# Kernel tuning notes

Measured on AMD Instinct MI355X. Metric: run time of the kernel, lower is better.

## Reference

```python
import jax, jax.numpy as jnp
import numpy as np

FP8_MAX = 448.0  # torch.finfo(float8_e4m3fn).max
TINY = float(np.finfo(np.float32).tiny)
BN = BK = 128  # block sizes


def _make_fp8_weight(key, N, K):
    """Mirror _create_fp8_weight: per-128x128-block scales, fp8 quantized values."""
    w = jax.random.normal(key, (N, K), jnp.float32) * 0.01
    wb = w.reshape(N // BN, BN, K // BK, BK)
    amax = jnp.abs(wb).max(axis=(1, 3))
    scale_inv = jnp.maximum(amax / FP8_MAX, TINY)  # [N/BN, K/BK]
    wq = (wb / scale_inv[:, None, :, None]).reshape(N, K)
    wq = wq.astype(jnp.float8_e4m3fn).astype(jnp.float32)  # fp8-rounded values
    return wq, scale_inv


def _dequant(wq, scale_inv):
    N, K = wq.shape
    nb, kb = scale_inv.shape
    wb = wq.reshape(nb, N // nb, kb, K // kb) * scale_inv[:, None, :, None]
    return wb.reshape(N, K)


def setup_inputs() -> dict:
    key = jax.random.key(0)
    kx, k1, k2, k3 = jax.random.split(key, 4)
    T, H, F = 4096, 2048, 7168  # tokens, hidden_dim, ffn_dim
    x = jax.random.normal(kx, (T, H), jnp.float32)
    w1_q, w1_s = _make_fp8_weight(k1, F, H)
    w3_q, w3_s = _make_fp8_weight(k3, F, H)
    w2_q, w2_s = _make_fp8_weight(k2, H, F)
    return {"hidden_states": x, "w1_q": w1_q, "w1_s": w1_s,
            "w3_q": w3_q, "w3_s": w3_s, "w2_q": w2_q, "w2_s": w2_s}


def reference(hidden_states, w1_q, w1_s, w3_q, w3_s, w2_q, w2_s):
    x = hidden_states
    w1 = _dequant(w1_q, w1_s)  # [F, H]
    w3 = _dequant(w3_q, w3_s)  # [F, H]
    w2 = _dequant(w2_q, w2_s)  # [H, F]
    g = x @ w1.T               # [T, F]
    u = x @ w3.T               # [T, F]
    fused = jax.nn.silu(g) * u
    return fused @ w2.T        # [T, H]
```

## Files before the change

### kernel.cpp

```cpp
#include <hip/hip_runtime.h>
#include <stdint.h>

typedef __attribute__((ext_vector_type(8))) short short8;
typedef __attribute__((ext_vector_type(4))) float floatx4;

__device__ __forceinline__ unsigned short f2bf(float f) {
  union { float f; unsigned int u; } c; c.f = f;
  unsigned int u = c.u;
  unsigned int r = (u + 0x7fffu + ((u >> 16) & 1u)) >> 16;
  return (unsigned short)r;
}
__device__ __forceinline__ float bf2f(unsigned short h) {
  union { unsigned int u; float f; } c; c.u = ((unsigned int)h) << 16;
  return c.f;
}

__device__ __forceinline__ void load16_to_lds(const void* g, void* l) {
  __builtin_amdgcn_global_load_lds(
      (const __attribute__((address_space(1))) unsigned int*)g,
      (__attribute__((address_space(3))) unsigned int*)l, 16, 0, 0);
}

__global__ void f32_to_bf16_kernel(const float* __restrict__ in,
                                   unsigned short* __restrict__ out, long n4) {
  long i = blockIdx.x * (long)blockDim.x + threadIdx.x;
  if (i >= n4) return;
  float4 v = ((const float4*)in)[i];
  ushort4 o;
  o.x = f2bf(v.x); o.y = f2bf(v.y); o.z = f2bf(v.z); o.w = f2bf(v.w);
  ((ushort4*)out)[i] = o;
}

__global__ void dequant2_kernel(const float* __restrict__ w1q,
                                const float* __restrict__ s1,
                                const float* __restrict__ w3q,
                                const float* __restrict__ s3,
                                unsigned short* __restrict__ o1,
                                unsigned short* __restrict__ o3,
                                int K, int sK) {
  int n = blockIdx.y;
  int k = blockIdx.x * 1024 + threadIdx.x * 4;
  size_t idx = (size_t)n * K + k;
  int sidx = (n >> 7) * sK + (k >> 7);
  float sc1 = s1[sidx], sc3 = s3[sidx];
  float4 v1 = *(const float4*)(w1q + idx);
  float4 v3 = *(const float4*)(w3q + idx);
  ushort4 a, b;
  a.x = f2bf(v1.x * sc1); a.y = f2bf(v1.y * sc1);
  a.z = f2bf(v1.z * sc1); a.w = f2bf(v1.w * sc1);
  b.x = f2bf(v3.x * sc3); b.y = f2bf(v3.y * sc3);
  b.z = f2bf(v3.z * sc3); b.w = f2bf(v3.w * sc3);
  *(ushort4*)(o1 + idx) = a;
  *(ushort4*)(o3 + idx) = b;
}

__global__ void dequant1_kernel(const float* __restrict__ wq,
                                const float* __restrict__ s,
                                unsigned short* __restrict__ out,
                                int K, int sK) {
  int n = blockIdx.y;
  int k = blockIdx.x * 1024 + threadIdx.x * 4;
  size_t idx = (size_t)n * K + k;
  float sc = s[(n >> 7) * sK + (k >> 7)];
  float4 v = *(const float4*)(wq + idx);
  ushort4 o;
  o.x = f2bf(v.x * sc); o.y = f2bf(v.y * sc);
  o.z = f2bf(v.z * sc); o.w = f2bf(v.w * sc);
  *(ushort4*)(out + idx) = o;
}


__global__ __launch_bounds__(512, 4) void dual_gemm_silu(
    const unsigned short* __restrict__ A,
    const unsigned short* __restrict__ B1,
    const unsigned short* __restrict__ B3,
    unsigned short* __restrict__ C,
    int M, int N, int K) {
  __shared__ unsigned short As[128 * 64];
  __shared__ unsigned short B1s[128 * 64];
  __shared__ unsigned short B3s[128 * 64];

  const int tid = threadIdx.x;
  const int lane = tid & 63;
  const int wave = tid >> 6;
  const int wm = wave >> 2;
  const int wn = wave & 3;
  const int m0 = blockIdx.y * 128, n0 = blockIdx.x * 128;

  const int s0 = tid, s1 = tid + 512;
  const int r0 = s0 >> 3, c0 = ((s0 & 7) ^ (r0 & 7)) * 8;
  const int r1 = s1 >> 3, c1 = ((s1 & 7) ^ (r1 & 7)) * 8;

  const int q = lane >> 4;
  const int r16 = lane & 15;
  const int rx = r16 & 7;

  floatx4 acc_g[4][2], acc_u[4][2];
#pragma unroll
  for (int i = 0; i < 4; i++)
#pragma unroll
    for (int j = 0; j < 2; j++) {
      acc_g[i][j] = (floatx4){0.f, 0.f, 0.f, 0.f};
      acc_u[i][j] = (floatx4){0.f, 0.f, 0.f, 0.f};
    }

  const unsigned short* ag0 = A + (size_t)(m0 + r0) * K + c0;
  const unsigned short* ag1 = A + (size_t)(m0 + r1) * K + c1;
  const unsigned short* b1g0 = B1 + (size_t)(n0 + r0) * K + c0;
  const unsigned short* b1g1 = B1 + (size_t)(n0 + r1) * K + c1;
  const unsigned short* b3g0 = B3 + (size_t)(n0 + r0) * K + c0;
  const unsigned short* b3g1 = B3 + (size_t)(n0 + r1) * K + c1;

  for (int k0 = 0; k0 < K; k0 += 64) {
    load16_to_lds(ag0 + k0, &As[s0 * 8]);
    load16_to_lds(ag1 + k0, &As[s1 * 8]);
    load16_to_lds(b1g0 + k0, &B1s[s0 * 8]);
    load16_to_lds(b1g1 + k0, &B1s[s1 * 8]);
    load16_to_lds(b3g0 + k0, &B3s[s0 * 8]);
    load16_to_lds(b3g1 + k0, &B3s[s1 * 8]);
    __syncthreads();

#pragma unroll
    for (int kh = 0; kh < 2; kh++) {
      const int kq = kh * 4 + q;
      short8 a[4], b1v[2], b3v[2];
#pragma unroll
      for (int t = 0; t < 4; t++) {
        int row = wm * 64 + t * 16 + r16;
        a[t] = *(const short8*)&As[(row * 8 + (kq ^ rx)) * 8];
      }
#pragma unroll
      for (int j = 0; j < 2; j++) {
        int row = wn * 32 + j * 16 + r16;
        int u = (row * 8 + (kq ^ rx)) * 8;
        b1v[j] = *(const short8*)&B1s[u];
        b3v[j] = *(const short8*)&B3s[u];
      }
#pragma unroll
      for (int i = 0; i < 4; i++)
#pragma unroll
        for (int j = 0; j < 2; j++) {
          acc_g[i][j] = __builtin_amdgcn_mfma_f32_16x16x32_bf16(
              a[i], b1v[j], acc_g[i][j], 0, 0, 0);
          acc_u[i][j] = __builtin_amdgcn_mfma_f32_16x16x32_bf16(
              a[i], b3v[j], acc_u[i][j], 0, 0, 0);
        }
    }
    __syncthreads();
  }

#pragma unroll
  for (int i = 0; i < 4; i++) {
    int row0 = m0 + wm * 64 + i * 16 + q * 4;
#pragma unroll
    for (int j = 0; j < 2; j++) {
      int col = n0 + wn * 32 + j * 16 + r16;
#pragma unroll
      for (int rr = 0; rr < 4; rr++) {
        float gv = acc_g[i][j][rr];
        float uv = acc_u[i][j][rr];
        float sv = gv / (1.f + __expf(-gv)) * uv;
        C[(size_t)(row0 + rr) * N + col] = f2bf(sv);
      }
    }
  }
}

__global__ __launch_bounds__(512, 4) void gemm_nt_f32_8w(
    const unsigned short* __restrict__ A,
    const unsigned short* __restrict__ B,
    float* __restrict__ C,
    int M, int N, int K) {
  __shared__ unsigned short As[128 * 64];
  __shared__ unsigned short Bs[128 * 64];

  const int tid = threadIdx.x;
  const int lane = tid & 63;
  const int wave = tid >> 6;
  const int wm = wave >> 2;
  const int wn = wave & 3;
  const int m0 = blockIdx.y * 128, n0 = blockIdx.x * 128;

  const int s0 = tid, s1 = tid + 512;
  const int r0 = s0 >> 3, c0 = ((s0 & 7) ^ (r0 & 7)) * 8;
  const int r1 = s1 >> 3, c1 = ((s1 & 7) ^ (r1 & 7)) * 8;

  const int q = lane >> 4;
  const int r16 = lane & 15;
  const int rx = r16 & 7;

  floatx4 acc[4][2];
#pragma unroll
  for (int i = 0; i < 4; i++)
#pragma unroll
    for (int j = 0; j < 2; j++) acc[i][j] = (floatx4){0.f, 0.f, 0.f, 0.f};

  const unsigned short* ag0 = A + (size_t)(m0 + r0) * K + c0;
  const unsigned short* ag1 = A + (size_t)(m0 + r1) * K + c1;
  const unsigned short* bg0 = B + (size_t)(n0 + r0) * K + c0;
  const unsigned short* bg1 = B + (size_t)(n0 + r1) * K + c1;

  for (int k0 = 0; k0 < K; k0 += 64) {
    load16_to_lds(ag0 + k0, &As[s0 * 8]);
    load16_to_lds(ag1 + k0, &As[s1 * 8]);
    load16_to_lds(bg0 + k0, &Bs[s0 * 8]);
    load16_to_lds(bg1 + k0, &Bs[s1 * 8]);
    __syncthreads();

#pragma unroll
    for (int kh = 0; kh < 2; kh++) {
      const int kq = kh * 4 + q;
      short8 a[4], b[2];
#pragma unroll
      for (int t = 0; t < 4; t++) {
        int row = wm * 64 + t * 16 + r16;
        a[t] = *(const short8*)&As[(row * 8 + (kq ^ rx)) * 8];
      }
#pragma unroll
      for (int j = 0; j < 2; j++) {
        int row = wn * 32 + j * 16 + r16;
        b[j] = *(const short8*)&Bs[(row * 8 + (kq ^ rx)) * 8];
      }
#pragma unroll
      for (int i = 0; i < 4; i++)
#pragma unroll
        for (int j = 0; j < 2; j++)
          acc[i][j] = __builtin_amdgcn_mfma_f32_16x16x32_bf16(
              a[i], b[j], acc[i][j], 0, 0, 0);
    }
    __syncthreads();
  }

#pragma unroll
  for (int i = 0; i < 4; i++) {
    int row0 = m0 + wm * 64 + i * 16 + q * 4;
#pragma unroll
    for (int j = 0; j < 2; j++) {
      int col = n0 + wn * 32 + j * 16 + r16;
#pragma unroll
      for (int rr = 0; rr < 4; rr++)
        C[(size_t)(row0 + rr) * N + col] = acc[i][j][rr];
    }
  }
}

extern "C" void kernel_launch(void* const* d_in, const int* in_sizes, int n_in,
                              void* d_out, int out_size, void* d_ws, size_t ws_size,
                              hipStream_t stream) {
  const float* x = (const float*)d_in[0];
  const float* w1q = (const float*)d_in[1];
  const float* w1s = (const float*)d_in[2];
  const float* w3q = (const float*)d_in[3];
  const float* w3s = (const float*)d_in[4];
  const float* w2q = (const float*)d_in[5];
  const float* w2s = (const float*)d_in[6];

  const int T = 4096, H = 2048, F = 7168;

  char* ws = (char*)d_ws;
  unsigned short* xb  = (unsigned short*)ws;  ws += (size_t)T * H * 2;
  unsigned short* w1b = (unsigned short*)ws;  ws += (size_t)F * H * 2;
  unsigned short* w3b = (unsigned short*)ws;  ws += (size_t)F * H * 2;
  unsigned short* w2b = (unsigned short*)ws;  ws += (size_t)H * F * 2;
  unsigned short* g   = (unsigned short*)ws;  ws += (size_t)T * F * 2;

  long xn4 = (long)T * H / 4;

  f32_to_bf16_kernel<<<(xn4 + 255) / 256, 256, 0, stream>>>(x, xb, xn4);
  dequant2_kernel<<<dim3(H / 1024, F), 256, 0, stream>>>(
      w1q, w1s, w3q, w3s, w1b, w3b, H, H / 128);
  dequant1_kernel<<<dim3(F / 1024, H), 256, 0, stream>>>(
      w2q, w2s, w2b, F, F / 128);

  dual_gemm_silu<<<dim3(F / 128, T / 128), 512, 0, stream>>>(xb, w1b, w3b, g, T, F, H);

  gemm_nt_f32_8w<<<dim3(H / 128, T / 128), 512, 0, stream>>>(g, w2b, (float*)d_out, T, H, F);
}
```

Before: 573.7 us.

## Use 4 waves per block with 64x64 warp tiles in both GEMMs

Both GEMM kernels drop from 8 waves to 4 waves per 128x128 block, so each wave computes a 64x64 sub-tile instead of 64x32. That doubles the MFMA work per B-fragment LDS read and cuts total LDS read traffic per block. Each thread now issues four global-to-LDS loads per matrix, using precomputed offsets. The cost is more accumulator registers per thread (32 floatx4 in the dual GEMM) and fewer waves per block to hide latency, with launch bounds lowered to 256 threads and 2 blocks.

```diff
diff --git a/kernel.cpp b/kernel.cpp
--- a/kernel.cpp
+++ b/kernel.cpp
@@ -70,7 +70,7 @@
 }
 
 
-__global__ __launch_bounds__(512, 4) void dual_gemm_silu(
+__global__ __launch_bounds__(256, 2) void dual_gemm_silu(
     const unsigned short* __restrict__ A,
     const unsigned short* __restrict__ B1,
     const unsigned short* __restrict__ B3,
@@ -83,55 +83,59 @@
   const int tid = threadIdx.x;
   const int lane = tid & 63;
   const int wave = tid >> 6;
-  const int wm = wave >> 2;
-  const int wn = wave & 3;
+  const int wm = wave >> 1;
+  const int wn = wave & 1;
   const int m0 = blockIdx.y * 128, n0 = blockIdx.x * 128;
 
-  const int s0 = tid, s1 = tid + 512;
-  const int r0 = s0 >> 3, c0 = ((s0 & 7) ^ (r0 & 7)) * 8;
-  const int r1 = s1 >> 3, c1 = ((s1 & 7) ^ (r1 & 7)) * 8;
+  int soff[4];
+  int sdst[4];
+#pragma unroll
+  for (int p = 0; p < 4; p++) {
+    int u = tid + 256 * p;
+    int r = u >> 3;
+    int c = ((u & 7) ^ (r & 7)) * 8;
+    soff[p] = r * K + c;
+    sdst[p] = u * 8;
+  }
 
   const int q = lane >> 4;
   const int r16 = lane & 15;
   const int rx = r16 & 7;
 
-  floatx4 acc_g[4][2], acc_u[4][2];
+  floatx4 acc_g[4][4], acc_u[4][4];
 #pragma unroll
   for (int i = 0; i < 4; i++)
 #pragma unroll
-    for (int j = 0; j < 2; j++) {
+    for (int j = 0; j < 4; j++) {
       acc_g[i][j] = (floatx4){0.f, 0.f, 0.f, 0.f};
       acc_u[i][j] = (floatx4){0.f, 0.f, 0.f, 0.f};
     }
 
-  const unsigned short* ag0 = A + (size_t)(m0 + r0) * K + c0;
-  const unsigned short* ag1 = A + (size_t)(m0 + r1) * K + c1;
-  const unsigned short* b1g0 = B1 + (size_t)(n0 + r0) * K + c0;
-  const unsigned short* b1g1 = B1 + (size_t)(n0 + r1) * K + c1;
-  const unsigned short* b3g0 = B3 + (size_t)(n0 + r0) * K + c0;
-  const unsigned short* b3g1 = B3 + (size_t)(n0 + r1) * K + c1;
+  const unsigned short* Abase = A + (size_t)m0 * K;
+  const unsigned short* B1base = B1 + (size_t)n0 * K;
+  const unsigned short* B3base = B3 + (size_t)n0 * K;
 
   for (int k0 = 0; k0 < K; k0 += 64) {
-    load16_to_lds(ag0 + k0, &As[s0 * 8]);
-    load16_to_lds(ag1 + k0, &As[s1 * 8]);
-    load16_to_lds(b1g0 + k0, &B1s[s0 * 8]);
-    load16_to_lds(b1g1 + k0, &B1s[s1 * 8]);
-    load16_to_lds(b3g0 + k0, &B3s[s0 * 8]);
-    load16_to_lds(b3g1 + k0, &B3s[s1 * 8]);
+#pragma unroll
+    for (int p = 0; p < 4; p++) {
+      load16_to_lds(Abase + soff[p] + k0, &As[sdst[p]]);
+      load16_to_lds(B1base + soff[p] + k0, &B1s[sdst[p]]);
+      load16_to_lds(B3base + soff[p] + k0, &B3s[sdst[p]]);
+    }
     __syncthreads();
 
 #pragma unroll
     for (int kh = 0; kh < 2; kh++) {
       const int kq = kh * 4 + q;
-      short8 a[4], b1v[2], b3v[2];
+      short8 a[4], b1v[4], b3v[4];
 #pragma unroll
       for (int t = 0; t < 4; t++) {
         int row = wm * 64 + t * 16 + r16;
         a[t] = *(const short8*)&As[(row * 8 + (kq ^ rx)) * 8];
       }
 #pragma unroll
-      for (int j = 0; j < 2; j++) {
-        int row = wn * 32 + j * 16 + r16;
+      for (int j = 0; j < 4; j++) {
+        int row = wn * 64 + j * 16 + r16;
         int u = (row * 8 + (kq ^ rx)) * 8;
         b1v[j] = *(const short8*)&B1s[u];
         b3v[j] = *(const short8*)&B3s[u];
@@ -139,7 +143,7 @@
 #pragma unroll
       for (int i = 0; i < 4; i++)
 #pragma unroll
-        for (int j = 0; j < 2; j++) {
+        for (int j = 0; j < 4; j++) {
           acc_g[i][j] = __builtin_amdgcn_mfma_f32_16x16x32_bf16(
               a[i], b1v[j], acc_g[i][j], 0, 0, 0);
           acc_u[i][j] = __builtin_amdgcn_mfma_f32_16x16x32_bf16(
@@ -153,8 +157,8 @@
   for (int i = 0; i < 4; i++) {
     int row0 = m0 + wm * 64 + i * 16 + q * 4;
 #pragma unroll
-    for (int j = 0; j < 2; j++) {
-      int col = n0 + wn * 32 + j * 16 + r16;
+    for (int j = 0; j < 4; j++) {
+      int col = n0 + wn * 64 + j * 16 + r16;
 #pragma unroll
       for (int rr = 0; rr < 4; rr++) {
         float gv = acc_g[i][j][rr];
@@ -166,7 +170,7 @@
   }
 }
 
-__global__ __launch_bounds__(512, 4) void gemm_nt_f32_8w(
+__global__ __launch_bounds__(256, 2) void gemm_nt_f32_4w(
     const unsigned short* __restrict__ A,
     const unsigned short* __restrict__ B,
     float* __restrict__ C,
@@ -177,54 +181,59 @@
   const int tid = threadIdx.x;
   const int lane = tid & 63;
   const int wave = tid >> 6;
-  const int wm = wave >> 2;
-  const int wn = wave & 3;
+  const int wm = wave >> 1;
+  const int wn = wave & 1;
   const int m0 = blockIdx.y * 128, n0 = blockIdx.x * 128;
 
-  const int s0 = tid, s1 = tid + 512;
-  const int r0 = s0 >> 3, c0 = ((s0 & 7) ^ (r0 & 7)) * 8;
-  const int r1 = s1 >> 3, c1 = ((s1 & 7) ^ (r1 & 7)) * 8;
+  int soff[4], sdst[4];
+#pragma unroll
+  for (int p = 0; p < 4; p++) {
+    int u = tid + 256 * p;
+    int r = u >> 3;
+    int c = ((u & 7) ^ (r & 7)) * 8;
+    soff[p] = r * K + c;
+    sdst[p] = u * 8;
+  }
 
   const int q = lane >> 4;
   const int r16 = lane & 15;
   const int rx = r16 & 7;
 
-  floatx4 acc[4][2];
+  floatx4 acc[4][4];
 #pragma unroll
   for (int i = 0; i < 4; i++)
 #pragma unroll
-    for (int j = 0; j < 2; j++) acc[i][j] = (floatx4){0.f, 0.f, 0.f, 0.f};
-
-  const unsigned short* ag0 = A + (size_t)(m0 + r0) * K + c0;
-  const unsigned short* ag1 = A + (size_t)(m0 + r1) * K + c1;
-  const unsigned short* bg0 = B + (size_t)(n0 + r0) * K + c0;
-  const unsigned short* bg1 = B + (size_t)(n0 + r1) * K + c1;
+    for (int j = 0; j < 4; j++) acc[i][j] = (floatx4){0.f, 0.f, 0.f, 0.f};
+
+  const unsigned short* Abase = A + (size_t)m0 * K;
+  const unsigned short* Bbase = B + (size_t)n0 * K;
 
   for (int k0 = 0; k0 < K; k0 += 64) {
-    load16_to_lds(ag0 + k0, &As[s0 * 8]);
-    load16_to_lds(ag1 + k0, &As[s1 * 8]);
-    load16_to_lds(bg0 + k0, &Bs[s0 * 8]);
-    load16_to_lds(bg1 + k0, &Bs[s1 * 8]);
+#pragma unroll
+    for (int p = 0; p < 4; p++) {
+      load16_to_lds(Abase + soff[p] + k0, &As[sdst[p]]);
+      load16_to_lds(Bbase + soff[p] + k0, &Bs[sdst[p]]);
+    }
     __syncthreads();
 
 #pragma unroll
     for (int kh = 0; kh < 2; kh++) {
       const int kq = kh * 4 + q;
-      short8 a[4], b[2];
+      short8 a[4], b[4];
 #pragma unroll
       for (int t = 0; t < 4; t++) {
         int row = wm * 64 + t * 16 + r16;
         a[t] = *(const short8*)&As[(row * 8 + (kq ^ rx)) * 8];
       }
 #pragma unroll
-      for (int j = 0; j < 2; j++) {
-        int row = wn * 32 + j * 16 + r16;
+      for (int j = 0; j < 4; j++) {
+        int row = wn * 64 + j * 16 + r16;
         b[j] = *(const short8*)&Bs[(row * 8 + (kq ^ rx)) * 8];
       }
 #pragma unroll
       for (int i = 0; i < 4; i++)
 #pragma unroll
-        for (int j = 0; j < 2; j++)
+        for (int j = 0; j < 4; j++)
           acc[i][j] = __builtin_amdgcn_mfma_f32_16x16x32_bf16(
               a[i], b[j], acc[i][j], 0, 0, 0);
     }
@@ -235,8 +244,8 @@
   for (int i = 0; i < 4; i++) {
     int row0 = m0 + wm * 64 + i * 16 + q * 4;
 #pragma unroll
-    for (int j = 0; j < 2; j++) {
-      int col = n0 + wn * 32 + j * 16 + r16;
+    for (int j = 0; j < 4; j++) {
+      int col = n0 + wn * 64 + j * 16 + r16;
 #pragma unroll
       for (int rr = 0; rr < 4; rr++)
         C[(size_t)(row0 + rr) * N + col] = acc[i][j][rr];
@@ -272,7 +281,7 @@
   dequant1_kernel<<<dim3(F / 1024, H), 256, 0, stream>>>(
       w2q, w2s, w2b, F, F / 128);
 
-  dual_gemm_silu<<<dim3(F / 128, T / 128), 512, 0, stream>>>(xb, w1b, w3b, g, T, F, H);
-
-  gemm_nt_f32_8w<<<dim3(H / 128, T / 128), 512, 0, stream>>>(g, w2b, (float*)d_out, T, H, F);
-}
+  dual_gemm_silu<<<dim3(F / 128, T / 128), 256, 0, stream>>>(xb, w1b, w3b, g, T, F, H);
+
+  gemm_nt_f32_4w<<<dim3(H / 128, T / 128), 256, 0, stream>>>(g, w2b, (float*)d_out, T, H, F);
+}
```

Result: faster. 562.0 us (-2.0%).
